# Performance work log

Hardware: AMD Instinct MI355X
Metric: run time of the kernel (lower is better)

## Reference

```python
import jax, jax.numpy as jnp
import numpy as np

PH = PW = 7          # pooled output size
SR = 2               # sampling_ratio: SR x SR samples per bin
SCALES = (0.25, 0.125, 0.0625, 0.03125)  # FPN strides 4,8,16,32
K = 512              # number of ROIs
B = 2                # batch (images)
IMG = 800.0


def _coords(start, bsize, P):
    # sample coords for P bins, SR samples per bin: start + p*bin + (i+0.5)*bin/SR
    j = jnp.arange(P * SR, dtype=start.dtype)
    return (start[:, None]
            + (j // SR)[None, :] * bsize[:, None]
            + ((j % SR) + 0.5)[None, :] * (bsize[:, None] / SR))  # [K, P*SR]


def _roi_align_level(feat, rois, scale):
    # feat: [B, C, H, W] ; rois: [K, 5] (batch_idx, x1, y1, x2, y2 in image coords)
    Bf, C, H, W = feat.shape
    b = rois[:, 0].astype(jnp.int32)
    x1 = rois[:, 1] * scale
    y1 = rois[:, 2] * scale
    x2 = rois[:, 3] * scale
    y2 = rois[:, 4] * scale
    roi_w = jnp.maximum(x2 - x1, 1.0)   # legacy (aligned=False) ROIAlign
    roi_h = jnp.maximum(y2 - y1, 1.0)
    ys = _coords(y1, roi_h / PH, PH)    # [K, Sy]
    xs = _coords(x1, roi_w / PW, PW)    # [K, Sx]
    y = ys[:, :, None]                  # [K, Sy, 1]
    x = xs[:, None, :]                  # [K, 1, Sx]
    valid = (y > -1.0) & (y < H) & (x > -1.0) & (x < W)  # [K, Sy, Sx]
    yc = jnp.clip(y, 0.0, None)
    xc = jnp.clip(x, 0.0, None)
    yl = jnp.minimum(yc.astype(jnp.int32), H - 1)
    xl = jnp.minimum(xc.astype(jnp.int32), W - 1)
    yh = jnp.minimum(yl + 1, H - 1)
    xh = jnp.minimum(xl + 1, W - 1)
    ly = jnp.where(yl >= H - 1, 0.0, yc - yl)
    lx = jnp.where(xl >= W - 1, 0.0, xc - xl)
    hy, hx = 1.0 - ly, 1.0 - lx
    feat_flat = feat.reshape(Bf, C, H * W)
    Sy, Sx = PH * SR, PW * SR
    acc = jnp.zeros((rois.shape[0], C, Sy, Sx), feat.dtype)
    corners = ((yl, xl, hy * hx), (yl, xh, hy * lx),
               (yh, xl, ly * hx), (yh, xh, ly * lx))
    for yy, xx, w in corners:  # fixed 4-corner loop (not a data-dim loop)
        idx = jnp.broadcast_to(yy * W + xx, (rois.shape[0], Sy, Sx))
        vals = jax.vmap(lambda bi, ii: jnp.take(feat_flat, bi, axis=0)[:, ii])(b, idx)
        acc = acc + vals * jnp.broadcast_to(w, idx.shape)[:, None, :, :]
    acc = jnp.where(valid[:, None, :, :], acc, 0.0)
    # average SRxSR samples within each 7x7 bin
    return acc.reshape(rois.shape[0], C, PH, SR, PW, SR).mean(axis=(3, 5))


def setup_inputs() -> dict:
    key = jax.random.key(0)
    ks = jax.random.split(key, 10)
    input_0 = jax.random.normal(ks[0], (B, 256, 200, 200), jnp.float32)
    input_1 = jax.random.normal(ks[1], (B, 256, 100, 100), jnp.float32)
    input_2 = jax.random.normal(ks[2], (B, 256, 50, 50), jnp.float32)
    input_3 = jax.random.normal(ks[3], (B, 256, 25, 25), jnp.float32)
    bidx = jax.random.randint(ks[4], (K,), 0, B).astype(jnp.float32)
    x1 = jax.random.uniform(ks[5], (K,)) * (IMG - 64.0)
    y1 = jax.random.uniform(ks[6], (K,)) * (IMG - 64.0)
    bw = 32.0 + jax.random.uniform(ks[7], (K,)) * 200.0
    bh = 32.0 + jax.random.uniform(ks[8], (K,)) * 200.0
    rois = jnp.stack([bidx, x1, y1,
                      jnp.minimum(x1 + bw, IMG),
                      jnp.minimum(y1 + bh, IMG)], axis=1).astype(jnp.float32)
    level = jax.random.randint(ks[9], (K,), 0, 4).astype(jnp.int32)
    rois_counts = jnp.array([K // 2, K - K // 2], jnp.int32)  # unused (all ROIs valid)
    return {"input_0": input_0, "input_1": input_1, "input_2": input_2,
            "input_3": input_3, "rois": rois, "rois_counts": rois_counts,
            "level": level}


def reference(input_0, input_1, input_2, input_3, rois, rois_counts, level):
    feats = (input_0, input_1, input_2, input_3)
    lvl = level.astype(jnp.int32)
    out = jnp.zeros((rois.shape[0], input_0.shape[1], PH, PW), input_0.dtype)
    for i, (f, s) in enumerate(zip(feats, SCALES)):
        o = _roi_align_level(f, rois, s)
        out = out + jnp.where((lvl == i)[:, None, None, None], o, 0.0)
    return out
```

## Files before the change

### kernel.cpp

```cpp
#include <hip/hip_runtime.h>


#define NUM_CH 256

typedef float floatx2 __attribute__((ext_vector_type(2)));

__global__ __launch_bounds__(256) void roi_align_kernel(
    const float* __restrict__ f0,
    const float* __restrict__ f1,
    const float* __restrict__ f2,
    const float* __restrict__ f3,
    const float* __restrict__ rois_f,
    const int* __restrict__ level,
    float* __restrict__ out,
    int total)
{
    int e = blockIdx.x * blockDim.x + threadIdx.x;
    if (e >= total) return;

    int p  = e % 49;
    int t  = e / 49;
    int c  = t % NUM_CH;
    int k  = t / NUM_CH;
    int ph = p / 7;
    int pw = p % 7;

    int lvl = level[k];
    const float* f;
    int H, W; float scale;
    if (lvl == 0)      { f = f0; H = 200; W = 200; scale = 0.25f;    }
    else if (lvl == 1) { f = f1; H = 100; W = 100; scale = 0.125f;   }
    else if (lvl == 2) { f = f2; H = 50;  W = 50;  scale = 0.0625f;  }
    else               { f = f3; H = 25;  W = 25;  scale = 0.03125f; }

    const float* rf = rois_f + (size_t)k * 5;
    float r0 = rf[0];
    float x1 = rf[1] * scale, y1 = rf[2] * scale;
    float x2 = rf[3] * scale, y2 = rf[4] * scale;
    int b = (int)r0;
    b = (b < 0) ? 0 : ((b > 1) ? 1 : b);

    float bh = fmaxf(y2 - y1, 1.0f) * (1.0f / 7.0f);
    float bw = fmaxf(x2 - x1, 1.0f) * (1.0f / 7.0f);

    const float* base = f + ((size_t)b * NUM_CH + c) * (size_t)(H * W);

    int   offA[4], offB[4];
    float selhi[4];
    float w00[4], w01[4], w10[4], w11[4];
    #pragma unroll
    for (int s = 0; s < 4; ++s) {
        int sy = s >> 1, sx = s & 1;
        float y = y1 + (float)ph * bh + ((float)sy + 0.5f) * (bh * 0.5f);
        float x = x1 + (float)pw * bw + ((float)sx + 0.5f) * (bw * 0.5f);
        bool valid = (y > -1.0f) && (y < (float)H) && (x > -1.0f) && (x < (float)W);
        float yc = fmaxf(y, 0.0f), xc = fmaxf(x, 0.0f);
        int yl = min((int)yc, H - 1);
        int yh = min(yl + 1, H - 1);
        int xl = min((int)xc, W - 1);
        float ly = (yl >= H - 1) ? 0.0f : (yc - (float)yl);
        float lx = (xl >= W - 1) ? 0.0f : (xc - (float)xl);
        float hy = 1.0f - ly, hx = 1.0f - lx;
        int xb = min(xl, W - 2);
        selhi[s] = (xl > xb) ? 1.0f : 0.0f;
        offA[s] = yl * W + xb;
        offB[s] = yh * W + xb;
        float vs = valid ? 0.25f : 0.0f;
        w00[s] = hy * hx * vs;
        w01[s] = hy * lx * vs;
        w10[s] = ly * hx * vs;
        w11[s] = ly * lx * vs;
    }

    floatx2 va[4], vb[4];
    #pragma unroll
    for (int s = 0; s < 4; ++s) {
        va[s] = *(const floatx2*)(base + offA[s]);
        vb[s] = *(const floatx2*)(base + offB[s]);
    }

    float acc = 0.0f;
    #pragma unroll
    for (int s = 0; s < 4; ++s) {
        float v00 = va[s].x + selhi[s] * (va[s].y - va[s].x);
        float v10 = vb[s].x + selhi[s] * (vb[s].y - vb[s].x);
        acc += w00[s] * v00 + w01[s] * va[s].y
             + w10[s] * v10 + w11[s] * vb[s].y;
    }

    out[e] = acc;
}

extern "C" void kernel_launch(void* const* d_in, const int* in_sizes, int n_in,
                              void* d_out, int out_size, void* d_ws, size_t ws_size,
                              hipStream_t stream) {
    const float* f0   = (const float*)d_in[0];
    const float* f1   = (const float*)d_in[1];
    const float* f2   = (const float*)d_in[2];
    const float* f3   = (const float*)d_in[3];
    const float* rois = (const float*)d_in[4];
    const int* level = (const int*)d_in[6];
    float* out = (float*)d_out;

    int total = out_size;
    int threads = 256;
    int blocks = (total + threads - 1) / threads;
    roi_align_kernel<<<blocks, threads, 0, stream>>>(f0, f1, f2, f3, rois, level, out, total);
}
```

Baseline: 186.9 us.

## Process two channels per thread, separate x/y sample math, swizzle blocks across XCDs

Each thread now computes two adjacent channels of the same ROI bin, so the coordinate and weight setup is shared and the thread issues twice as many independent gathers. The y and x sample parameters are computed separately and combined, which cuts redundant per-sample arithmetic. Block indices are remapped so that consecutive logical blocks land on the same XCD, which may improve L2 locality on the feature maps. In exchange there are half as many threads, more registers per thread, and output writes become strided by 49 floats between the two channels.

```diff
diff --git a/kernel.cpp b/kernel.cpp
--- a/kernel.cpp
+++ b/kernel.cpp
@@ -15,15 +15,24 @@
     float* __restrict__ out,
     int total)
 {
-    int e = blockIdx.x * blockDim.x + threadIdx.x;
+    int b = blockIdx.x;
+    int nb = gridDim.x;
+    int wb = b;
+    if ((nb & 7) == 0) {
+        int per = nb >> 3;
+        wb = (b & 7) * per + (b >> 3);
+    }
+
+    int e = wb * 256 + threadIdx.x;
     if (e >= total) return;
 
     int p  = e % 49;
     int t  = e / 49;
-    int c  = t % NUM_CH;
-    int k  = t / NUM_CH;
+    int cp = t % (NUM_CH / 2);
+    int k  = t / (NUM_CH / 2);
     int ph = p / 7;
     int pw = p % 7;
+    int c0 = cp * 2;
 
     int lvl = level[k];
     const float* f;
@@ -37,58 +46,81 @@
     float r0 = rf[0];
     float x1 = rf[1] * scale, y1 = rf[2] * scale;
     float x2 = rf[3] * scale, y2 = rf[4] * scale;
-    int b = (int)r0;
-    b = (b < 0) ? 0 : ((b > 1) ? 1 : b);
+    int bi = (int)r0;
+    bi = (bi < 0) ? 0 : ((bi > 1) ? 1 : bi);
 
     float bh = fmaxf(y2 - y1, 1.0f) * (1.0f / 7.0f);
     float bw = fmaxf(x2 - x1, 1.0f) * (1.0f / 7.0f);
 
-    const float* base = f + ((size_t)b * NUM_CH + c) * (size_t)(H * W);
+    const size_t HW = (size_t)(H * W);
+    const float* base0 = f + ((size_t)bi * NUM_CH + c0) * HW;
 
-    int   offA[4], offB[4];
-    float selhi[4];
-    float w00[4], w01[4], w10[4], w11[4];
+    int   rA[2], rB[2];
+    float lyv[2], hyv[2], vy[2];
+    #pragma unroll
+    for (int sy = 0; sy < 2; ++sy) {
+        float y = y1 + (float)ph * bh + ((float)sy + 0.5f) * (bh * 0.5f);
+        bool valid = (y > -1.0f) && (y < (float)H);
+        float yc = fmaxf(y, 0.0f);
+        int yl = min((int)yc, H - 1);
+        int yh = min(yl + 1, H - 1);
+        float ly = (yl >= H - 1) ? 0.0f : (yc - (float)yl);
+        rA[sy] = yl * W;
+        rB[sy] = yh * W;
+        lyv[sy] = ly; hyv[sy] = 1.0f - ly;
+        vy[sy] = valid ? 0.25f : 0.0f;
+    }
+    int   xb[2];
+    float lxv[2], hxv[2], sel[2], vx[2];
+    #pragma unroll
+    for (int sx = 0; sx < 2; ++sx) {
+        float x = x1 + (float)pw * bw + ((float)sx + 0.5f) * (bw * 0.5f);
+        bool valid = (x > -1.0f) && (x < (float)W);
+        float xc = fmaxf(x, 0.0f);
+        int xl = min((int)xc, W - 1);
+        float lx = (xl >= W - 1) ? 0.0f : (xc - (float)xl);
+        int xq = min(xl, W - 2);
+        xb[sx] = xq;
+        sel[sx] = (xl > xq) ? 1.0f : 0.0f;
+        lxv[sx] = lx; hxv[sx] = 1.0f - lx;
+        vx[sx] = valid ? 1.0f : 0.0f;
+    }
+
+    floatx2 va0[4], vb0[4], va1[4], vb1[4];
     #pragma unroll
     for (int s = 0; s < 4; ++s) {
         int sy = s >> 1, sx = s & 1;
-        float y = y1 + (float)ph * bh + ((float)sy + 0.5f) * (bh * 0.5f);
-        float x = x1 + (float)pw * bw + ((float)sx + 0.5f) * (bw * 0.5f);
-        bool valid = (y > -1.0f) && (y < (float)H) && (x > -1.0f) && (x < (float)W);
-        float yc = fmaxf(y, 0.0f), xc = fmaxf(x, 0.0f);
-        int yl = min((int)yc, H - 1);
-        int yh = min(yl + 1, H - 1);
-        int xl = min((int)xc, W - 1);
-        float ly = (yl >= H - 1) ? 0.0f : (yc - (float)yl);
-        float lx = (xl >= W - 1) ? 0.0f : (xc - (float)xl);
-        float hy = 1.0f - ly, hx = 1.0f - lx;
-        int xb = min(xl, W - 2);
-        selhi[s] = (xl > xb) ? 1.0f : 0.0f;
-        offA[s] = yl * W + xb;
-        offB[s] = yh * W + xb;
-        float vs = valid ? 0.25f : 0.0f;
-        w00[s] = hy * hx * vs;
-        w01[s] = hy * lx * vs;
-        w10[s] = ly * hx * vs;
-        w11[s] = ly * lx * vs;
+        int oA = rA[sy] + xb[sx];
+        int oB = rB[sy] + xb[sx];
+        va0[s] = *(const floatx2*)(base0 + oA);
+        vb0[s] = *(const floatx2*)(base0 + oB);
+        va1[s] = *(const floatx2*)(base0 + HW + oA);
+        vb1[s] = *(const floatx2*)(base0 + HW + oB);
     }
 
-    floatx2 va[4], vb[4];
+    float acc0 = 0.0f, acc1 = 0.0f;
     #pragma unroll
     for (int s = 0; s < 4; ++s) {
-        va[s] = *(const floatx2*)(base + offA[s]);
-        vb[s] = *(const floatx2*)(base + offB[s]);
+        int sy = s >> 1, sx = s & 1;
+        float vs  = vy[sy] * vx[sx];
+        float w00 = hyv[sy] * hxv[sx] * vs;
+        float w01 = hyv[sy] * lxv[sx] * vs;
+        float w10 = lyv[sy] * hxv[sx] * vs;
+        float w11 = lyv[sy] * lxv[sx] * vs;
+        float s0  = sel[sx];
+
+        float a00 = va0[s].x + s0 * (va0[s].y - va0[s].x);
+        float a10 = vb0[s].x + s0 * (vb0[s].y - vb0[s].x);
+        acc0 += w00 * a00 + w01 * va0[s].y + w10 * a10 + w11 * vb0[s].y;
+
+        float b00 = va1[s].x + s0 * (va1[s].y - va1[s].x);
+        float b10 = vb1[s].x + s0 * (vb1[s].y - vb1[s].x);
+        acc1 += w00 * b00 + w01 * va1[s].y + w10 * b10 + w11 * vb1[s].y;
     }
 
-    float acc = 0.0f;
-    #pragma unroll
-    for (int s = 0; s < 4; ++s) {
-        float v00 = va[s].x + selhi[s] * (va[s].y - va[s].x);
-        float v10 = vb[s].x + selhi[s] * (vb[s].y - vb[s].x);
-        acc += w00[s] * v00 + w01[s] * va[s].y
-             + w10[s] * v10 + w11[s] * vb[s].y;
-    }
-
-    out[e] = acc;
+    size_t ob = ((size_t)k * NUM_CH + c0) * 49 + p;
+    out[ob]      = acc0;
+    out[ob + 49] = acc1;
 }
 
 extern "C" void kernel_launch(void* const* d_in, const int* in_sizes, int n_in,
@@ -102,7 +134,7 @@
     const int* level = (const int*)d_in[6];
     float* out = (float*)d_out;
 
-    int total = out_size;
+    int total = out_size / 2;
     int threads = 256;
     int blocks = (total + threads - 1) / threads;
     roi_align_kernel<<<blocks, threads, 0, stream>>>(f0, f1, f2, f3, rois, level, out, total);
```

After: 200.9 us. 1.07x slower.
